# Kernel optimization log

Measured on AMD Instinct MI355X. Metric: run time of the kernel, lower is better.

## Reference

```python
import jax, jax.numpy as jnp
import numpy as np

T, J, D = 8192, 1024, 256  # context len, query len, 2*hidden


def setup_inputs() -> dict:
    key = jax.random.key(0)
    k1, k2, k3 = jax.random.split(key, 3)
    context = jax.random.normal(k1, (T, D), dtype=jnp.float32)
    query = jax.random.normal(k2, (J, D), dtype=jnp.float32)
    # sim_weight: Linear(3*D, 1, bias=False) -> single weight vector of length 3*D
    w = jax.random.normal(k3, (3 * D,), dtype=jnp.float32) * (1.0 / np.sqrt(3 * D))
    return {"context": context, "query": query, "w": w}


def reference(context, query, w):
    D = context.shape[1]
    # Decompose w.[c; q; c*q] into three rank-1 / matmul terms instead of
    # materializing [T,J,3D] concatenated pairs.
    w_c, w_q, w_m = w[:D], w[D:2 * D], w[2 * D:]
    # S[t,j] = c_t.w_c + q_j.w_q + (c_t * w_m).q_j   -> [T, J]
    S = (context @ w_c)[:, None] + (query @ w_q)[None, :] + (context * w_m) @ query.T
    # context-to-query attention: softmax over query positions j
    A = jax.nn.softmax(S, axis=1)                    # [T, J]
    context2query = A @ query                        # [T, D]
    # NOTE: original code takes b = max_j S (no softmax over t) and
    # h_tilde = sum_t b[t] * c_t  (a single [D] vector)
    b = jnp.max(S, axis=1)                           # [T]
    h_tilde = b @ context                            # [D]
    # G[t] = [c_t; c2q_t; c_t*c2q_t; c_t*h_tilde]    -> [T, 4D]
    G = jnp.concatenate(
        [context, context2query, context * context2query, context * h_tilde[None, :]],
        axis=1,
    )
    return G
```

## Files before the change

kernel.cpp:

```cpp
#include <hip/hip_runtime.h>
#include <stdint.h>

#define T_DIM 8192
#define J_DIM 1024
#define D_DIM 256

typedef __bf16 bf16x8 __attribute__((ext_vector_type(8)));
typedef float f32x4 __attribute__((ext_vector_type(4)));
typedef unsigned short u16x8 __attribute__((ext_vector_type(8)));
typedef unsigned short u16x4 __attribute__((ext_vector_type(4)));

__device__ inline unsigned short f2bf(float x) {
    unsigned u = __builtin_bit_cast(unsigned, x);
    u += 0x7FFFu + ((u >> 16) & 1u);
    return (unsigned short)(u >> 16);
}

__device__ inline void gll16(const void* g, void* l) {
    __builtin_amdgcn_global_load_lds(
        (const __attribute__((address_space(1))) unsigned int*)g,
        (__attribute__((address_space(3))) unsigned int*)l, 16, 0, 0);
}

__global__ __launch_bounds__(256) void prep_all(const float* __restrict__ ctx,
                                                const float* __restrict__ qry,
                                                const float* __restrict__ w,
                                                unsigned short* __restrict__ Cm,
                                                float* __restrict__ cw,
                                                unsigned short* __restrict__ Qb,
                                                unsigned short* __restrict__ QT,
                                                float* __restrict__ qw,
                                                float* __restrict__ stats) {
    int wid = threadIdx.x >> 6, lane = threadIdx.x & 63;
    if (blockIdx.x >= 2304) {
        int idx = (blockIdx.x - 2304) * 256 + threadIdx.x;
        if (idx < 2 * T_DIM + D_DIM) stats[idx] = 0.0f;
        return;
    }
    if (blockIdx.x < 2048) {
        int t = blockIdx.x * 4 + wid;
        float4 c  = *(const float4*)(ctx + (size_t)t * D_DIM + lane * 4);
        float4 wm = *(const float4*)(w + 2 * D_DIM + lane * 4);
        float4 wc = *(const float4*)(w + lane * 4);
        u16x4 cmv;
        cmv[0] = f2bf(c.x * wm.x);
        cmv[1] = f2bf(c.y * wm.y);
        cmv[2] = f2bf(c.z * wm.z);
        cmv[3] = f2bf(c.w * wm.w);
        *(u16x4*)(Cm + (size_t)t * D_DIM + lane * 4) = cmv;
        float s = c.x * wc.x + c.y * wc.y + c.z * wc.z + c.w * wc.w;
        #pragma unroll
        for (int o = 1; o < 64; o <<= 1) s += __shfl_xor(s, o);
        if (lane == 0) cw[t] = s;
    } else {
        int j = (blockIdx.x - 2048) * 4 + wid;
        float4 c  = *(const float4*)(qry + (size_t)j * D_DIM + lane * 4);
        float4 wq = *(const float4*)(w + D_DIM + lane * 4);
        u16x4 qv;
        qv[0] = f2bf(c.x);
        qv[1] = f2bf(c.y);
        qv[2] = f2bf(c.z);
        qv[3] = f2bf(c.w);
        *(u16x4*)(Qb + (size_t)j * D_DIM + lane * 4) = qv;
        int d0 = lane * 4;
        QT[(size_t)(d0 + 0) * J_DIM + j] = qv[0];
        QT[(size_t)(d0 + 1) * J_DIM + j] = qv[1];
        QT[(size_t)(d0 + 2) * J_DIM + j] = qv[2];
        QT[(size_t)(d0 + 3) * J_DIM + j] = qv[3];
        float s = c.x * wq.x + c.y * wq.y + c.z * wq.z + c.w * wq.w;
        #pragma unroll
        for (int o = 1; o < 64; o <<= 1) s += __shfl_xor(s, o);
        if (lane == 0) qw[j] = s;
    }
}

__global__ __launch_bounds__(256) void gemm_s(const unsigned short* __restrict__ Cm,
                                              const unsigned short* __restrict__ Qb,
                                              const float* __restrict__ qw,
                                              unsigned short* __restrict__ P,
                                              float* __restrict__ lsum,
                                              int* __restrict__ rmax) {
    __shared__ unsigned short SH[12288];
    __shared__ float statS[2][64];
    __shared__ float statM[2][64];
    unsigned short* As = SH;
    unsigned short* Bs = SH + 4096;
    int tid = threadIdx.x, lane = tid & 63, wv = tid >> 6;
    int wm = wv >> 1, wn = wv & 1;
    int bm = blockIdx.x & 127, bn = blockIdx.x >> 7;
    int cidx = lane & 15, rgrp = lane >> 4;
    int srow8 = lane >> 3;
    int swzc = (lane & 7) ^ srow8;
    f32x4 acc[2][4] = {};

    const unsigned short* Asrc = Cm + (size_t)(bm * 64 + srow8) * 256 + (swzc << 3);
    const unsigned short* Bsrc = Qb + (size_t)(bn * 128 + srow8) * 256 + (swzc << 3);

    for (int k0 = 0; k0 < 256; k0 += 64) {
        if (k0) __syncthreads();
        #pragma unroll
        for (int i = 0; i < 2; ++i) {
            int g = wv * 2 + i;
            gll16(Asrc + (size_t)(g * 8) * 256 + k0, As + g * 512);
        }
        #pragma unroll
        for (int i = 0; i < 4; ++i) {
            int g = wv * 4 + i;
            gll16(Bsrc + (size_t)(g * 8) * 256 + k0, Bs + g * 512);
        }
        __syncthreads();
        #pragma unroll
        for (int ks = 0; ks < 2; ++ks) {
            int klo = ks * 4 + rgrp;
            bf16x8 af[2], bfr[4];
            #pragma unroll
            for (int m = 0; m < 2; ++m) {
                int ra = wm * 32 + m * 16 + cidx;
                af[m] = __builtin_bit_cast(bf16x8,
                        *(const u16x8*)(As + ra * 64 + ((klo ^ (ra & 7)) << 3)));
            }
            #pragma unroll
            for (int n = 0; n < 4; ++n) {
                int rb = wn * 64 + n * 16 + cidx;
                bfr[n] = __builtin_bit_cast(bf16x8,
                        *(const u16x8*)(Bs + rb * 64 + ((klo ^ (rb & 7)) << 3)));
            }
            #pragma unroll
            for (int m = 0; m < 2; ++m)
                #pragma unroll
                for (int n = 0; n < 4; ++n)
                    acc[m][n] = __builtin_amdgcn_mfma_f32_16x16x32_bf16(af[m], bfr[n], acc[m][n], 0, 0, 0);
        }
    }

    float qwv[4];
    #pragma unroll
    for (int n = 0; n < 4; ++n) qwv[n] = qw[bn * 128 + wn * 64 + n * 16 + cidx];
    #pragma unroll
    for (int m = 0; m < 2; ++m) {
        #pragma unroll
        for (int rg = 0; rg < 4; ++rg) {
            float s = 0.f, mx = 0.f;
            #pragma unroll
            for (int n = 0; n < 4; ++n) {
                float p = __expf(acc[m][n][rg] + qwv[n]);
                acc[m][n][rg] = p;
                s += p;
                mx = fmaxf(mx, p);
            }
            #pragma unroll
            for (int o = 1; o < 16; o <<= 1) {
                s += __shfl_xor(s, o);
                mx = fmaxf(mx, __shfl_xor(mx, o));
            }
            if (cidx == 0) {
                int row = wm * 32 + m * 16 + rgrp * 4 + rg;
                statS[wn][row] = s;
                statM[wn][row] = mx;
            }
        }
    }
    __syncthreads();
    if (tid < 64) {
        atomicAdd(lsum + bm * 64 + tid, statS[0][tid] + statS[1][tid]);
        atomicMax(rmax + bm * 64 + tid,
                  __float_as_int(fmaxf(statM[0][tid], statM[1][tid])));
    }

    #pragma unroll
    for (int m = 0; m < 2; ++m)
        #pragma unroll
        for (int n = 0; n < 4; ++n)
            #pragma unroll
            for (int rg = 0; rg < 4; ++rg) {
                int row = wm * 32 + m * 16 + rgrp * 4 + rg;
                int col = wn * 64 + n * 16 + cidx;
                SH[row * 128 + (((col >> 3) ^ (row & 7)) << 3) + (col & 7)] = f2bf(acc[m][n][rg]);
            }
    __syncthreads();
    #pragma unroll
    for (int i = 0; i < 4; ++i) {
        int r = i * 16 + (tid >> 4);
        int c8 = tid & 15;
        u16x8 v = *(const u16x8*)(SH + r * 128 + ((c8 ^ (r & 7)) << 3));
        *(u16x8*)(P + (size_t)(bm * 64 + r) * J_DIM + bn * 128 + c8 * 8) = v;
    }
}

__global__ __launch_bounds__(256) void hb_kernel(const float* __restrict__ rmaxf,
                                                 const float* __restrict__ cw,
                                                 const float* __restrict__ ctx,
                                                 float* __restrict__ ht) {
    __shared__ float bsh[64];
    int tid = threadIdx.x;
    int t0b = blockIdx.x * 64;
    if (tid < 64) bsh[tid] = __logf(rmaxf[t0b + tid]) + cw[t0b + tid];
    __syncthreads();
    float pb = 0.f;
    #pragma unroll 8
    for (int r = 0; r < 64; ++r)
        pb += bsh[r] * ctx[(size_t)(t0b + r) * D_DIM + tid];
    atomicAdd(ht + tid, pb);
}

__global__ __launch_bounds__(256) void gemm_o(const unsigned short* __restrict__ P,
                                              const unsigned short* __restrict__ QT,
                                              const float* __restrict__ lsum,
                                              const float* __restrict__ ht,
                                              const float* __restrict__ ctx,
                                              float* __restrict__ G) {
    __shared__ unsigned short SH[8192];
    unsigned short* As = SH;
    unsigned short* Bs = SH + 4096;
    float* SH32 = (float*)SH;
    int tid = threadIdx.x, lane = tid & 63, wv = tid >> 6;
    int wm = wv >> 1, wn = wv & 1;
    int bm = blockIdx.x & 127, bn = blockIdx.x >> 7;
    int cidx = lane & 15, rgrp = lane >> 4;
    int srow8 = lane >> 3;
    int swzc = (lane & 7) ^ srow8;
    f32x4 acc[2][2] = {};

    const unsigned short* Ap = P  + (size_t)(bm * 64 + srow8) * J_DIM + (swzc << 3);
    const unsigned short* Bp = QT + (size_t)(bn * 64 + srow8) * J_DIM + (swzc << 3);

    for (int k0 = 0; k0 < 1024; k0 += 64) {
        if (k0) __syncthreads();
        #pragma unroll
        for (int i = 0; i < 2; ++i) {
            int g = wv * 2 + i;
            gll16(Ap + (size_t)(g * 8) * J_DIM + k0, As + g * 512);
        }
        #pragma unroll
        for (int i = 0; i < 2; ++i) {
            int g = wv * 2 + i;
            gll16(Bp + (size_t)(g * 8) * J_DIM + k0, Bs + g * 512);
        }
        __syncthreads();
        #pragma unroll
        for (int ks = 0; ks < 2; ++ks) {
            int klo = ks * 4 + rgrp;
            bf16x8 af[2], bfr[2];
            #pragma unroll
            for (int m = 0; m < 2; ++m) {
                int ra = wm * 32 + m * 16 + cidx;
                af[m] = __builtin_bit_cast(bf16x8,
                        *(const u16x8*)(As + ra * 64 + ((klo ^ (ra & 7)) << 3)));
            }
            #pragma unroll
            for (int n = 0; n < 2; ++n) {
                int rb = wn * 32 + n * 16 + cidx;
                bfr[n] = __builtin_bit_cast(bf16x8,
                        *(const u16x8*)(Bs + rb * 64 + ((klo ^ (rb & 7)) << 3)));
            }
            #pragma unroll
            for (int m = 0; m < 2; ++m)
                #pragma unroll
                for (int n = 0; n < 2; ++n)
                    acc[m][n] = __builtin_amdgcn_mfma_f32_16x16x32_bf16(af[m], bfr[n], acc[m][n], 0, 0, 0);
        }
    }

    __syncthreads();
    #pragma unroll
    for (int i = 0; i < 4; ++i) {
        int idx = tid + i * 256;
        int row = idx >> 4, c4 = idx & 15;
        int t = bm * 64 + row;
        int d = bn * 64 + c4 * 4;
        float4 c = *(const float4*)(ctx + (size_t)t * D_DIM + d);
        float4 h = *(const float4*)(ht + d);
        float* gr = G + (size_t)t * 1024;
        *(float4*)(gr + d) = c;
        float4 o3;
        o3.x = c.x * h.x; o3.y = c.y * h.y; o3.z = c.z * h.z; o3.w = c.w * h.w;
        *(float4*)(gr + 768 + d) = o3;
    }
    #pragma unroll
    for (int m = 0; m < 2; ++m) {
        #pragma unroll
        for (int rg = 0; rg < 4; ++rg) {
            int row = wm * 32 + m * 16 + rgrp * 4 + rg;
            float linv = 1.0f / lsum[bm * 64 + row];
            #pragma unroll
            for (int n = 0; n < 2; ++n) {
                int col = wn * 32 + n * 16 + cidx;
                int c4 = col >> 2, slot = c4 ^ (row & 15);
                SH32[row * 64 + slot * 4 + (col & 3)] = acc[m][n][rg] * linv;
            }
        }
    }
    __syncthreads();
    #pragma unroll
    for (int i = 0; i < 4; ++i) {
        int idx = tid + i * 256;
        int row = idx >> 4, c4 = idx & 15;
        int slot = c4 ^ (row & 15);
        float4 v = *(const float4*)(SH32 + row * 64 + slot * 4);
        int t = bm * 64 + row;
        int d = bn * 64 + c4 * 4;
        float4 c = *(const float4*)(ctx + (size_t)t * D_DIM + d);
        float* gr = G + (size_t)t * 1024;
        *(float4*)(gr + 256 + d) = v;
        float4 o2;
        o2.x = c.x * v.x; o2.y = c.y * v.y; o2.z = c.z * v.z; o2.w = c.w * v.w;
        *(float4*)(gr + 512 + d) = o2;
    }
}

extern "C" void kernel_launch(void* const* d_in, const int* in_sizes, int n_in,
                              void* d_out, int out_size, void* d_ws, size_t ws_size,
                              hipStream_t stream) {
    (void)in_sizes; (void)n_in; (void)out_size; (void)ws_size;
    const float* ctx = (const float*)d_in[0];
    const float* qry = (const float*)d_in[1];
    const float* w   = (const float*)d_in[2];
    float* G = (float*)d_out;
    char* ws = (char*)d_ws;

    constexpr size_t OFF_P  = 0;
    constexpr size_t OFF_CM = OFF_P  + (size_t)T_DIM * J_DIM * 2;
    constexpr size_t OFF_QB = OFF_CM + (size_t)T_DIM * D_DIM * 2;
    constexpr size_t OFF_QT = OFF_QB + (size_t)J_DIM * D_DIM * 2;
    constexpr size_t OFF_CW = OFF_QT + (size_t)D_DIM * J_DIM * 2;
    constexpr size_t OFF_QW = OFF_CW + (size_t)T_DIM * 4;
    constexpr size_t OFF_ST = OFF_QW + (size_t)J_DIM * 4;

    unsigned short* P  = (unsigned short*)(ws + OFF_P);
    unsigned short* Cm = (unsigned short*)(ws + OFF_CM);
    unsigned short* Qb = (unsigned short*)(ws + OFF_QB);
    unsigned short* QT = (unsigned short*)(ws + OFF_QT);
    float* cw    = (float*)(ws + OFF_CW);
    float* qw    = (float*)(ws + OFF_QW);
    float* stats = (float*)(ws + OFF_ST);
    float* lsum  = stats;
    float* rmax  = stats + T_DIM;
    float* ht    = stats + 2 * T_DIM;

    prep_all<<<dim3(2369), 256, 0, stream>>>(ctx, qry, w, Cm, cw, Qb, QT, qw, stats);
    gemm_s<<<dim3(1024), 256, 0, stream>>>(Cm, Qb, qw, P, lsum, (int*)rmax);
    hb_kernel<<<dim3(128), 256, 0, stream>>>(rmax, cw, ctx, ht);
    gemm_o<<<dim3(512), 256, 0, stream>>>(P, QT, lsum, ht, ctx, G);
}
```

Measured before the change: 47.83 us.

## Fuse score GEMM, h_tilde reduction and output GEMM into one kernel with flag sync

```diff
diff --git a/kernel.cpp b/kernel.cpp
--- a/kernel.cpp
+++ b/kernel.cpp
@@ -34,7 +34,7 @@
     int wid = threadIdx.x >> 6, lane = threadIdx.x & 63;
     if (blockIdx.x >= 2304) {
         int idx = (blockIdx.x - 2304) * 256 + threadIdx.x;
-        if (idx < 2 * T_DIM + D_DIM) stats[idx] = 0.0f;
+        if (idx < 2 * T_DIM + D_DIM + 129) stats[idx] = 0.0f;
         return;
     }
     if (blockIdx.x < 2048) {
@@ -74,237 +74,267 @@
     }
 }
 
-__global__ __launch_bounds__(256) void gemm_s(const unsigned short* __restrict__ Cm,
-                                              const unsigned short* __restrict__ Qb,
-                                              const float* __restrict__ qw,
-                                              unsigned short* __restrict__ P,
-                                              float* __restrict__ lsum,
-                                              int* __restrict__ rmax) {
-    __shared__ unsigned short SH[12288];
-    __shared__ float statS[2][64];
-    __shared__ float statM[2][64];
-    unsigned short* As = SH;
-    unsigned short* Bs = SH + 4096;
+__global__ __launch_bounds__(256) void mega_gemm(const unsigned short* __restrict__ Cm,
+                                                 const unsigned short* __restrict__ Qb,
+                                                 const float* __restrict__ qw,
+                                                 const unsigned short* __restrict__ QT,
+                                                 const float* __restrict__ cw,
+                                                 const float* __restrict__ ctx,
+                                                 unsigned short* __restrict__ P,
+                                                 float* __restrict__ lsum,
+                                                 int* __restrict__ rmax,
+                                                 float* __restrict__ ht,
+                                                 unsigned int* __restrict__ done,
+                                                 unsigned int* __restrict__ htdone,
+                                                 float* __restrict__ G) {
+    __shared__ char RAW[25600];
     int tid = threadIdx.x, lane = tid & 63, wv = tid >> 6;
-    int wm = wv >> 1, wn = wv & 1;
-    int bm = blockIdx.x & 127, bn = blockIdx.x >> 7;
-    int cidx = lane & 15, rgrp = lane >> 4;
-    int srow8 = lane >> 3;
-    int swzc = (lane & 7) ^ srow8;
-    f32x4 acc[2][4] = {};
-
-    const unsigned short* Asrc = Cm + (size_t)(bm * 64 + srow8) * 256 + (swzc << 3);
-    const unsigned short* Bsrc = Qb + (size_t)(bn * 128 + srow8) * 256 + (swzc << 3);
-
-    for (int k0 = 0; k0 < 256; k0 += 64) {
-        if (k0) __syncthreads();
-        #pragma unroll
-        for (int i = 0; i < 2; ++i) {
-            int g = wv * 2 + i;
-            gll16(Asrc + (size_t)(g * 8) * 256 + k0, As + g * 512);
-        }
+
+    if (blockIdx.x < 1024) {
+        unsigned short* SH = (unsigned short*)RAW;
+        unsigned short* As = SH;
+        unsigned short* Bs = SH + 4096;
+        float* statS0 = (float*)(RAW + 24576);
+        float* statS1 = statS0 + 64;
+        float* statM0 = statS1 + 64;
+        float* statM1 = statM0 + 64;
+        int wm = wv >> 1, wn = wv & 1;
+        int bm = blockIdx.x & 127, bn = blockIdx.x >> 7;
+        int cidx = lane & 15, rgrp = lane >> 4;
+        int srow8 = lane >> 3;
+        int swzc = (lane & 7) ^ srow8;
+        f32x4 acc[2][4] = {};
+
+        const unsigned short* Asrc = Cm + (size_t)(bm * 64 + srow8) * 256 + (swzc << 3);
+        const unsigned short* Bsrc = Qb + (size_t)(bn * 128 + srow8) * 256 + (swzc << 3);
+
+        for (int k0 = 0; k0 < 256; k0 += 64) {
+            if (k0) __syncthreads();
+            #pragma unroll
+            for (int i = 0; i < 2; ++i) {
+                int g = wv * 2 + i;
+                gll16(Asrc + (size_t)(g * 8) * 256 + k0, As + g * 512);
+            }
+            #pragma unroll
+            for (int i = 0; i < 4; ++i) {
+                int g = wv * 4 + i;
+                gll16(Bsrc + (size_t)(g * 8) * 256 + k0, Bs + g * 512);
+            }
+            __syncthreads();
+            #pragma unroll
+            for (int ks = 0; ks < 2; ++ks) {
+                int klo = ks * 4 + rgrp;
+                bf16x8 af[2], bfr[4];
+                #pragma unroll
+                for (int m = 0; m < 2; ++m) {
+                    int ra = wm * 32 + m * 16 + cidx;
+                    af[m] = __builtin_bit_cast(bf16x8,
+                            *(const u16x8*)(As + ra * 64 + ((klo ^ (ra & 7)) << 3)));
+                }
+                #pragma unroll
+                for (int n = 0; n < 4; ++n) {
+                    int rb = wn * 64 + n * 16 + cidx;
+                    bfr[n] = __builtin_bit_cast(bf16x8,
+                            *(const u16x8*)(Bs + rb * 64 + ((klo ^ (rb & 7)) << 3)));
+                }
+                #pragma unroll
+                for (int m = 0; m < 2; ++m)
+                    #pragma unroll
+                    for (int n = 0; n < 4; ++n)
+                        acc[m][n] = __builtin_amdgcn_mfma_f32_16x16x32_bf16(af[m], bfr[n], acc[m][n], 0, 0, 0);
+            }
+        }
+
+        float qwv[4];
+        #pragma unroll
+        for (int n = 0; n < 4; ++n) qwv[n] = qw[bn * 128 + wn * 64 + n * 16 + cidx];
+        #pragma unroll
+        for (int m = 0; m < 2; ++m) {
+            #pragma unroll
+            for (int rg = 0; rg < 4; ++rg) {
+                float s = 0.f, mx = 0.f;
+                #pragma unroll
+                for (int n = 0; n < 4; ++n) {
+                    float p = __expf(acc[m][n][rg] + qwv[n]);
+                    acc[m][n][rg] = p;
+                    s += p;
+                    mx = fmaxf(mx, p);
+                }
+                #pragma unroll
+                for (int o = 1; o < 16; o <<= 1) {
+                    s += __shfl_xor(s, o);
+                    mx = fmaxf(mx, __shfl_xor(mx, o));
+                }
+                if (cidx == 0) {
+                    int row = wm * 32 + m * 16 + rgrp * 4 + rg;
+                    (wn ? statS1 : statS0)[row] = s;
+                    (wn ? statM1 : statM0)[row] = mx;
+                }
+            }
+        }
+        __syncthreads();
+        if (tid < 64) {
+            atomicAdd(lsum + bm * 64 + tid, statS0[tid] + statS1[tid]);
+            atomicMax(rmax + bm * 64 + tid,
+                      __float_as_int(fmaxf(statM0[tid], statM1[tid])));
+        }
+
+        #pragma unroll
+        for (int m = 0; m < 2; ++m)
+            #pragma unroll
+            for (int n = 0; n < 4; ++n)
+                #pragma unroll
+                for (int rg = 0; rg < 4; ++rg) {
+                    int row = wm * 32 + m * 16 + rgrp * 4 + rg;
+                    int col = wn * 64 + n * 16 + cidx;
+                    SH[row * 128 + (((col >> 3) ^ (row & 7)) << 3) + (col & 7)] = f2bf(acc[m][n][rg]);
+                }
+        __syncthreads();
         #pragma unroll
         for (int i = 0; i < 4; ++i) {
-            int g = wv * 4 + i;
-            gll16(Bsrc + (size_t)(g * 8) * 256 + k0, Bs + g * 512);
-        }
-        __syncthreads();
-        #pragma unroll
-        for (int ks = 0; ks < 2; ++ks) {
-            int klo = ks * 4 + rgrp;
-            bf16x8 af[2], bfr[4];
-            #pragma unroll
-            for (int m = 0; m < 2; ++m) {
-                int ra = wm * 32 + m * 16 + cidx;
-                af[m] = __builtin_bit_cast(bf16x8,
-                        *(const u16x8*)(As + ra * 64 + ((klo ^ (ra & 7)) << 3)));
-            }
-            #pragma unroll
-            for (int n = 0; n < 4; ++n) {
-                int rb = wn * 64 + n * 16 + cidx;
-                bfr[n] = __builtin_bit_cast(bf16x8,
-                        *(const u16x8*)(Bs + rb * 64 + ((klo ^ (rb & 7)) << 3)));
-            }
-            #pragma unroll
-            for (int m = 0; m < 2; ++m)
-                #pragma unroll
-                for (int n = 0; n < 4; ++n)
-                    acc[m][n] = __builtin_amdgcn_mfma_f32_16x16x32_bf16(af[m], bfr[n], acc[m][n], 0, 0, 0);
-        }
-    }
-
-    float qwv[4];
-    #pragma unroll
-    for (int n = 0; n < 4; ++n) qwv[n] = qw[bn * 128 + wn * 64 + n * 16 + cidx];
-    #pragma unroll
-    for (int m = 0; m < 2; ++m) {
-        #pragma unroll
-        for (int rg = 0; rg < 4; ++rg) {
-            float s = 0.f, mx = 0.f;
-            #pragma unroll
-            for (int n = 0; n < 4; ++n) {
-                float p = __expf(acc[m][n][rg] + qwv[n]);
-                acc[m][n][rg] = p;
-                s += p;
-                mx = fmaxf(mx, p);
-            }
-            #pragma unroll
-            for (int o = 1; o < 16; o <<= 1) {
-                s += __shfl_xor(s, o);
-                mx = fmaxf(mx, __shfl_xor(mx, o));
-            }
-            if (cidx == 0) {
-                int row = wm * 32 + m * 16 + rgrp * 4 + rg;
-                statS[wn][row] = s;
-                statM[wn][row] = mx;
-            }
-        }
-    }
-    __syncthreads();
-    if (tid < 64) {
-        atomicAdd(lsum + bm * 64 + tid, statS[0][tid] + statS[1][tid]);
-        atomicMax(rmax + bm * 64 + tid,
-                  __float_as_int(fmaxf(statM[0][tid], statM[1][tid])));
-    }
-
-    #pragma unroll
-    for (int m = 0; m < 2; ++m)
-        #pragma unroll
-        for (int n = 0; n < 4; ++n)
+            int r = i * 16 + (tid >> 4);
+            int c8 = tid & 15;
+            u16x8 v = *(const u16x8*)(SH + r * 128 + ((c8 ^ (r & 7)) << 3));
+            *(u16x8*)(P + (size_t)(bm * 64 + r) * J_DIM + bn * 128 + c8 * 8) = v;
+        }
+        asm volatile("s_waitcnt vmcnt(0)" ::: "memory");
+        __syncthreads();
+        if (tid == 0)
+            __hip_atomic_fetch_add(&done[bm], 1u, __ATOMIC_RELEASE, __HIP_MEMORY_SCOPE_AGENT);
+        return;
+    }
+
+    if (blockIdx.x < 1152) {
+        float* bsh = (float*)RAW;
+        int stripe = blockIdx.x - 1024;
+        if (tid == 0) {
+            while (__hip_atomic_load(&done[stripe], __ATOMIC_ACQUIRE, __HIP_MEMORY_SCOPE_AGENT) < 8u)
+                __builtin_amdgcn_s_sleep(1);
+        }
+        __syncthreads();
+        int t0b = stripe * 64;
+        if (tid < 64)
+            bsh[tid] = __logf(__int_as_float(rmax[t0b + tid])) + cw[t0b + tid];
+        __syncthreads();
+        float pb = 0.f;
+        #pragma unroll 8
+        for (int r = 0; r < 64; ++r)
+            pb += bsh[r] * ctx[(size_t)(t0b + r) * D_DIM + tid];
+        atomicAdd(ht + tid, pb);
+        __syncthreads();
+        if (tid == 0)
+            __hip_atomic_fetch_add(htdone, 1u, __ATOMIC_RELEASE, __HIP_MEMORY_SCOPE_AGENT);
+        return;
+    }
+
+    {
+        unsigned short* As = (unsigned short*)RAW;
+        unsigned short* Bs = As + 4096;
+        float* SH32 = (float*)RAW;
+        int obid = blockIdx.x - 1152;
+        int wm = wv >> 1, wn = wv & 1;
+        int bm = obid & 127, bn = obid >> 7;
+        int cidx = lane & 15, rgrp = lane >> 4;
+        int srow8 = lane >> 3;
+        int swzc = (lane & 7) ^ srow8;
+        f32x4 acc[2][2] = {};
+
+        if (tid == 0) {
+            while (__hip_atomic_load(&done[bm], __ATOMIC_ACQUIRE, __HIP_MEMORY_SCOPE_AGENT) < 8u)
+                __builtin_amdgcn_s_sleep(1);
+        }
+        __syncthreads();
+
+        const unsigned short* Ap = P  + (size_t)(bm * 64 + srow8) * J_DIM + (swzc << 3);
+        const unsigned short* Bp = QT + (size_t)(bn * 64 + srow8) * J_DIM + (swzc << 3);
+
+        for (int k0 = 0; k0 < 1024; k0 += 64) {
+            if (k0) __syncthreads();
+            #pragma unroll
+            for (int i = 0; i < 2; ++i) {
+                int g = wv * 2 + i;
+                gll16(Ap + (size_t)(g * 8) * J_DIM + k0, As + g * 512);
+            }
+            #pragma unroll
+            for (int i = 0; i < 2; ++i) {
+                int g = wv * 2 + i;
+                gll16(Bp + (size_t)(g * 8) * J_DIM + k0, Bs + g * 512);
+            }
+            __syncthreads();
+            #pragma unroll
+            for (int ks = 0; ks < 2; ++ks) {
+                int klo = ks * 4 + rgrp;
+                bf16x8 af[2], bfr[2];
+                #pragma unroll
+                for (int m = 0; m < 2; ++m) {
+                    int ra = wm * 32 + m * 16 + cidx;
+                    af[m] = __builtin_bit_cast(bf16x8,
+                            *(const u16x8*)(As + ra * 64 + ((klo ^ (ra & 7)) << 3)));
+                }
+                #pragma unroll
+                for (int n = 0; n < 2; ++n) {
+                    int rb = wn * 32 + n * 16 + cidx;
+                    bfr[n] = __builtin_bit_cast(bf16x8,
+                            *(const u16x8*)(Bs + rb * 64 + ((klo ^ (rb & 7)) << 3)));
+                }
+                #pragma unroll
+                for (int m = 0; m < 2; ++m)
+                    #pragma unroll
+                    for (int n = 0; n < 2; ++n)
+                        acc[m][n] = __builtin_amdgcn_mfma_f32_16x16x32_bf16(af[m], bfr[n], acc[m][n], 0, 0, 0);
+            }
+        }
+
+        if (tid == 0) {
+            while (__hip_atomic_load(htdone, __ATOMIC_ACQUIRE, __HIP_MEMORY_SCOPE_AGENT) < 128u)
+                __builtin_amdgcn_s_sleep(1);
+        }
+        __syncthreads();
+
+        #pragma unroll
+        for (int i = 0; i < 4; ++i) {
+            int idx = tid + i * 256;
+            int row = idx >> 4, c4 = idx & 15;
+            int t = bm * 64 + row;
+            int d = bn * 64 + c4 * 4;
+            float4 c = *(const float4*)(ctx + (size_t)t * D_DIM + d);
+            float4 h = *(const float4*)(ht + d);
+            float* gr = G + (size_t)t * 1024;
+            *(float4*)(gr + d) = c;
+            float4 o3;
+            o3.x = c.x * h.x; o3.y = c.y * h.y; o3.z = c.z * h.z; o3.w = c.w * h.w;
+            *(float4*)(gr + 768 + d) = o3;
+        }
+        #pragma unroll
+        for (int m = 0; m < 2; ++m) {
             #pragma unroll
             for (int rg = 0; rg < 4; ++rg) {
                 int row = wm * 32 + m * 16 + rgrp * 4 + rg;
-                int col = wn * 64 + n * 16 + cidx;
-                SH[row * 128 + (((col >> 3) ^ (row & 7)) << 3) + (col & 7)] = f2bf(acc[m][n][rg]);
-            }
-    __syncthreads();
-    #pragma unroll
-    for (int i = 0; i < 4; ++i) {
-        int r = i * 16 + (tid >> 4);
-        int c8 = tid & 15;
-        u16x8 v = *(const u16x8*)(SH + r * 128 + ((c8 ^ (r & 7)) << 3));
-        *(u16x8*)(P + (size_t)(bm * 64 + r) * J_DIM + bn * 128 + c8 * 8) = v;
-    }
-}
-
-__global__ __launch_bounds__(256) void hb_kernel(const float* __restrict__ rmaxf,
-                                                 const float* __restrict__ cw,
-                                                 const float* __restrict__ ctx,
-                                                 float* __restrict__ ht) {
-    __shared__ float bsh[64];
-    int tid = threadIdx.x;
-    int t0b = blockIdx.x * 64;
-    if (tid < 64) bsh[tid] = __logf(rmaxf[t0b + tid]) + cw[t0b + tid];
-    __syncthreads();
-    float pb = 0.f;
-    #pragma unroll 8
-    for (int r = 0; r < 64; ++r)
-        pb += bsh[r] * ctx[(size_t)(t0b + r) * D_DIM + tid];
-    atomicAdd(ht + tid, pb);
-}
-
-__global__ __launch_bounds__(256) void gemm_o(const unsigned short* __restrict__ P,
-                                              const unsigned short* __restrict__ QT,
-                                              const float* __restrict__ lsum,
-                                              const float* __restrict__ ht,
-                                              const float* __restrict__ ctx,
-                                              float* __restrict__ G) {
-    __shared__ unsigned short SH[8192];
-    unsigned short* As = SH;
-    unsigned short* Bs = SH + 4096;
-    float* SH32 = (float*)SH;
-    int tid = threadIdx.x, lane = tid & 63, wv = tid >> 6;
-    int wm = wv >> 1, wn = wv & 1;
-    int bm = blockIdx.x & 127, bn = blockIdx.x >> 7;
-    int cidx = lane & 15, rgrp = lane >> 4;
-    int srow8 = lane >> 3;
-    int swzc = (lane & 7) ^ srow8;
-    f32x4 acc[2][2] = {};
-
-    const unsigned short* Ap = P  + (size_t)(bm * 64 + srow8) * J_DIM + (swzc << 3);
-    const unsigned short* Bp = QT + (size_t)(bn * 64 + srow8) * J_DIM + (swzc << 3);
-
-    for (int k0 = 0; k0 < 1024; k0 += 64) {
-        if (k0) __syncthreads();
-        #pragma unroll
-        for (int i = 0; i < 2; ++i) {
-            int g = wv * 2 + i;
-            gll16(Ap + (size_t)(g * 8) * J_DIM + k0, As + g * 512);
-        }
-        #pragma unroll
-        for (int i = 0; i < 2; ++i) {
-            int g = wv * 2 + i;
-            gll16(Bp + (size_t)(g * 8) * J_DIM + k0, Bs + g * 512);
-        }
-        __syncthreads();
-        #pragma unroll
-        for (int ks = 0; ks < 2; ++ks) {
-            int klo = ks * 4 + rgrp;
-            bf16x8 af[2], bfr[2];
-            #pragma unroll
-            for (int m = 0; m < 2; ++m) {
-                int ra = wm * 32 + m * 16 + cidx;
-                af[m] = __builtin_bit_cast(bf16x8,
-                        *(const u16x8*)(As + ra * 64 + ((klo ^ (ra & 7)) << 3)));
-            }
-            #pragma unroll
-            for (int n = 0; n < 2; ++n) {
-                int rb = wn * 32 + n * 16 + cidx;
-                bfr[n] = __builtin_bit_cast(bf16x8,
-                        *(const u16x8*)(Bs + rb * 64 + ((klo ^ (rb & 7)) << 3)));
-            }
-            #pragma unroll
-            for (int m = 0; m < 2; ++m)
-                #pragma unroll
-                for (int n = 0; n < 2; ++n)
-                    acc[m][n] = __builtin_amdgcn_mfma_f32_16x16x32_bf16(af[m], bfr[n], acc[m][n], 0, 0, 0);
-        }
-    }
-
-    __syncthreads();
-    #pragma unroll
-    for (int i = 0; i < 4; ++i) {
-        int idx = tid + i * 256;
-        int row = idx >> 4, c4 = idx & 15;
-        int t = bm * 64 + row;
-        int d = bn * 64 + c4 * 4;
-        float4 c = *(const float4*)(ctx + (size_t)t * D_DIM + d);
-        float4 h = *(const float4*)(ht + d);
-        float* gr = G + (size_t)t * 1024;
-        *(float4*)(gr + d) = c;
-        float4 o3;
-        o3.x = c.x * h.x; o3.y = c.y * h.y; o3.z = c.z * h.z; o3.w = c.w * h.w;
-        *(float4*)(gr + 768 + d) = o3;
-    }
-    #pragma unroll
-    for (int m = 0; m < 2; ++m) {
-        #pragma unroll
-        for (int rg = 0; rg < 4; ++rg) {
-            int row = wm * 32 + m * 16 + rgrp * 4 + rg;
-            float linv = 1.0f / lsum[bm * 64 + row];
-            #pragma unroll
-            for (int n = 0; n < 2; ++n) {
-                int col = wn * 32 + n * 16 + cidx;
-                int c4 = col >> 2, slot = c4 ^ (row & 15);
-                SH32[row * 64 + slot * 4 + (col & 3)] = acc[m][n][rg] * linv;
-            }
-        }
-    }
-    __syncthreads();
-    #pragma unroll
-    for (int i = 0; i < 4; ++i) {
-        int idx = tid + i * 256;
-        int row = idx >> 4, c4 = idx & 15;
-        int slot = c4 ^ (row & 15);
-        float4 v = *(const float4*)(SH32 + row * 64 + slot * 4);
-        int t = bm * 64 + row;
-        int d = bn * 64 + c4 * 4;
-        float4 c = *(const float4*)(ctx + (size_t)t * D_DIM + d);
-        float* gr = G + (size_t)t * 1024;
-        *(float4*)(gr + 256 + d) = v;
-        float4 o2;
-        o2.x = c.x * v.x; o2.y = c.y * v.y; o2.z = c.z * v.z; o2.w = c.w * v.w;
-        *(float4*)(gr + 512 + d) = o2;
+                float linv = 1.0f / lsum[bm * 64 + row];
+                #pragma unroll
+                for (int n = 0; n < 2; ++n) {
+                    int col = wn * 32 + n * 16 + cidx;
+                    int c4 = col >> 2, slot = c4 ^ (row & 15);
+                    SH32[row * 64 + slot * 4 + (col & 3)] = acc[m][n][rg] * linv;
+                }
+            }
+        }
+        __syncthreads();
+        #pragma unroll
+        for (int i = 0; i < 4; ++i) {
+            int idx = tid + i * 256;
+            int row = idx >> 4, c4 = idx & 15;
+            int slot = c4 ^ (row & 15);
+            float4 v = *(const float4*)(SH32 + row * 64 + slot * 4);
+            int t = bm * 64 + row;
+            int d = bn * 64 + c4 * 4;
+            float4 c = *(const float4*)(ctx + (size_t)t * D_DIM + d);
+            float* gr = G + (size_t)t * 1024;
+            *(float4*)(gr + 256 + d) = v;
+            float4 o2;
+            o2.x = c.x * v.x; o2.y = c.y * v.y; o2.z = c.z * v.z; o2.w = c.w * v.w;
+            *(float4*)(gr + 512 + d) = o2;
+        }
     }
 }
 
@@ -336,9 +366,10 @@
     float* lsum  = stats;
     float* rmax  = stats + T_DIM;
     float* ht    = stats + 2 * T_DIM;
-
-    prep_all<<<dim3(2369), 256, 0, stream>>>(ctx, qry, w, Cm, cw, Qb, QT, qw, stats);
-    gemm_s<<<dim3(1024), 256, 0, stream>>>(Cm, Qb, qw, P, lsum, (int*)rmax);
-    hb_kernel<<<dim3(128), 256, 0, stream>>>(rmax, cw, ctx, ht);
-    gemm_o<<<dim3(512), 256, 0, stream>>>(P, QT, lsum, ht, ctx, G);
-}
+    unsigned int* done   = (unsigned int*)(stats + 2 * T_DIM + D_DIM);
+    unsigned int* htdone = (unsigned int*)(stats + 2 * T_DIM + D_DIM + 128);
+
+    prep_all<<<dim3(2370), 256, 0, stream>>>(ctx, qry, w, Cm, cw, Qb, QT, qw, stats);
+    mega_gemm<<<dim3(1664), 256, 0, stream>>>(Cm, Qb, qw, QT, cw, ctx, P,
+                                              lsum, (int*)rmax, ht, done, htdone, G);
+}
```

Measured after the change: 104.9 us. +119.3%, slower.
